# Optimization experiments

Hardware: AMD Instinct MI355X
Metric: run time of the kernel (lower is better)

The kernel has to match this reference:

```python
import jax, jax.numpy as jnp
import numpy as np


def setup_inputs() -> dict:
    key = jax.random.key(0)
    kq, kk, kv = jax.random.split(key, 3)
    B, S, D = 4, 4096, 64
    q = jax.random.normal(kq, (B, S, D), dtype=jnp.float32)
    k = jax.random.normal(kk, (B, S, D), dtype=jnp.float32)
    v = jax.random.normal(kv, (B, S, D), dtype=jnp.float32)
    return {"q": q, "k": k, "v": v}


def reference(q, k, v):
    # Faithful math of the original blocked loop:
    #   output_i += exp(Q_i @ K_j^T) @ V_j, summed over all column blocks j
    # which is exactly unnormalized exponential attention:
    #   out = exp(Q K^T) V  (no 1/sqrt(d) scaling, no softmax normalization,
    #   no max-subtraction -- matching the source module's math).
    scores = jnp.einsum("bqd,bkd->bqk", q, k)  # [B, Sq, Sk]
    return jnp.einsum("bqk,bkd->bqd", jnp.exp(scores), v)  # [B, Sq, D]
```

## Files before the change

kernel.cpp:

```cpp
#include <hip/hip_runtime.h>
#include <hip/hip_bf16.h>


typedef short    s16x4 __attribute__((ext_vector_type(4)));
typedef short    s16x8 __attribute__((ext_vector_type(8)));
typedef _Float16 h16x8 __attribute__((ext_vector_type(8)));
typedef float    fx4   __attribute__((ext_vector_type(4)));
typedef float    fx16  __attribute__((ext_vector_type(16)));

constexpr int S = 4096, D = 64, BN = 128;
constexpr int TILES = S / BN;
constexpr int HALF_TILES = TILES / 2;
constexpr int TILE_SHORTS  = 16 * 512;
constexpr int BATCH_SHORTS = TILES * TILE_SHORTS;

__device__ __forceinline__ unsigned short f2bf(float x) {
    unsigned u = __float_as_uint(x);
    u = (u + 0x7FFFu + ((u >> 16) & 1u)) >> 16;
    return (unsigned short)u;
}
__device__ __forceinline__ float bf2f(unsigned short h) {
    return __uint_as_float(((unsigned)h) << 16);
}
__device__ __forceinline__ unsigned short f2h(float x) {
    union { _Float16 h; unsigned short s; } u;
    u.h = (_Float16)x;
    return u.s;
}
__device__ __forceinline__ unsigned pack_bf16(float lo, float hi) {
    __hip_bfloat162 r = __float22bfloat162_rn(make_float2(lo, hi));
    union { __hip_bfloat162 b; unsigned u; } c;
    c.b = r;
    return c.u;
}
__device__ __forceinline__ float ex2(float x) {
#if __has_builtin(__builtin_amdgcn_exp2f)
    return __builtin_amdgcn_exp2f(x);
#else
    return exp2f(x);
#endif
}

__global__ __launch_bounds__(256) void prep2(
    const float* __restrict__ k, const float* __restrict__ v,
    unsigned short* __restrict__ kf, unsigned short* __restrict__ vf)
{
    __shared__ unsigned short tile[128 * 72];
    const int tid   = threadIdx.x;
    const int which = blockIdx.x & 1;
    const int t     = (blockIdx.x >> 1) & 31;
    const int b     = blockIdx.x >> 6;
    const float* src = (which ? v : k) + ((size_t)b * S + t * BN) * D;

    #pragma unroll
    for (int i = 0; i < 8; ++i) {
        int f   = i * 256 + tid;
        int row = f >> 4;
        int c4  = (f & 15) << 2;
        float4 x = *(const float4*)(src + row * D + c4);
        s16x4 o;
        if (which) o = (s16x4){(short)f2bf(x.x), (short)f2bf(x.y),
                               (short)f2bf(x.z), (short)f2bf(x.w)};
        else       o = (s16x4){(short)f2h(x.x), (short)f2h(x.y),
                               (short)f2h(x.z), (short)f2h(x.w)};
        *(s16x4*)&tile[row * 72 + c4] = o;
    }
    __syncthreads();

    const int lane = tid & 63;
    unsigned short* dst = (which ? vf : kf) + (size_t)b * BATCH_SHORTS + t * TILE_SHORTS;
    #pragma unroll
    for (int i = 0; i < 4; ++i) {
        int c = (tid >> 6) * 4 + i;
        s16x8 o;
        if (which == 0) {
            int row = (c >> 2) * 32 + (lane & 31);
            int dc  = (c & 3) * 16 + (lane >> 5) * 8;
            o = *(const s16x8*)&tile[row * 72 + dc];
        } else {
            int r0 = (c >> 1) * 16 + (lane >> 5) * 8;
            int dc = (c & 1) * 32 + (lane & 31);
            #pragma unroll
            for (int j = 0; j < 8; ++j) o[j] = (short)tile[(r0 + j) * 72 + dc];
        }
        *(s16x8*)(dst + c * 512 + lane * 8) = o;
    }
}

__global__ __launch_bounds__(512) void attn_main10(
    const float* __restrict__ q, const unsigned short* __restrict__ kf,
    const unsigned short* __restrict__ vf, float* __restrict__ partial)
{
    const int tid = threadIdx.x, lane = tid & 63, w = tid >> 6;
    const int h = lane >> 5, m5 = lane & 31;
    const int bid = blockIdx.x;
    const int kslice = bid & 7;
    const int kh = kslice >> 2;
    const int kkq = kslice & 3;
    const int rest = bid >> 3;
    const int b = rest & 3;
    const int q0 = (rest >> 2) * 512 + w * 64;
    const int t0 = kh * HALF_TILES;

    const unsigned short* kwb = kf + (size_t)b * BATCH_SHORTS + kkq * 4 * 512 + lane * 8;
    const unsigned short* vwb = vf + (size_t)b * BATCH_SHORTS + kkq * 4 * 512 + lane * 8;

    const float LOG2E = 1.4426950408889634f;
    h16x8 qf[2][4];
    #pragma unroll
    for (int mt = 0; mt < 2; ++mt) {
        const float* qrow = q + ((size_t)b * S + q0 + mt * 32 + m5) * D + h * 8;
        #pragma unroll
        for (int ks = 0; ks < 4; ++ks) {
            float4 a = *(const float4*)(qrow + ks * 16);
            float4 c = *(const float4*)(qrow + ks * 16 + 4);
            qf[mt][ks] = (h16x8){
                (_Float16)(a.x * LOG2E), (_Float16)(a.y * LOG2E),
                (_Float16)(a.z * LOG2E), (_Float16)(a.w * LOG2E),
                (_Float16)(c.x * LOG2E), (_Float16)(c.y * LOG2E),
                (_Float16)(c.z * LOG2E), (_Float16)(c.w * LOG2E)};
        }
    }

    fx16 oacc[2][2] = {};

    h16x8 kA0[4], kA1[4];
    s16x8 vB0[4], vB1[4];

    auto loadKV = [&](int t, h16x8* kA, s16x8* vB) {
        const unsigned short* kt = kwb + (size_t)t * TILE_SHORTS;
        const unsigned short* vt = vwb + (size_t)t * TILE_SHORTS;
        #pragma unroll
        for (int c = 0; c < 4; ++c) {
            kA[c] = *(const h16x8*)(kt + c * 512);
            vB[c] = *(const s16x8*)(vt + c * 512);
        }
    };

    auto computeTile = [&](const h16x8* kA, const s16x8* vB) {
        fx16 sa[2] = {};
        #pragma unroll
        for (int ks = 0; ks < 4; ++ks)
            #pragma unroll
            for (int mt = 0; mt < 2; ++mt)
                sa[mt] = __builtin_amdgcn_mfma_f32_32x32x16_f16(kA[ks], qf[mt][ks], sa[mt], 0, 0, 0);

        unsigned p01[2][8];
        #pragma unroll
        for (int mt = 0; mt < 2; ++mt)
            #pragma unroll
            for (int rp = 0; rp < 8; ++rp)
                p01[mt][rp] = pack_bf16(ex2(sa[mt][2 * rp]), ex2(sa[mt][2 * rp + 1]));

        union frag { unsigned u[4]; s16x8 v; };
        frag A[2][2];
        #pragma unroll
        for (int mt = 0; mt < 2; ++mt) {
#if __has_builtin(__builtin_amdgcn_permlane32_swap)
            typedef unsigned uix2 __attribute__((ext_vector_type(2)));
            uix2 r0 = __builtin_amdgcn_permlane32_swap(p01[mt][0], p01[mt][2], false, false);
            uix2 r1 = __builtin_amdgcn_permlane32_swap(p01[mt][1], p01[mt][3], false, false);
            A[mt][0].u[0] = r0.x; A[mt][0].u[1] = r1.x;
            A[mt][0].u[2] = r0.y; A[mt][0].u[3] = r1.y;
            uix2 r2 = __builtin_amdgcn_permlane32_swap(p01[mt][4], p01[mt][6], false, false);
            uix2 r3 = __builtin_amdgcn_permlane32_swap(p01[mt][5], p01[mt][7], false, false);
            A[mt][1].u[0] = r2.x; A[mt][1].u[1] = r3.x;
            A[mt][1].u[2] = r2.y; A[mt][1].u[3] = r3.y;
#else
            unsigned sw[8];
            #pragma unroll
            for (int rp = 0; rp < 8; ++rp)
                sw[rp] = (unsigned)__shfl_xor((int)p01[mt][rp], 32, 64);
            A[mt][0].u[0] = h ? sw[2]        : p01[mt][0];
            A[mt][0].u[1] = h ? sw[3]        : p01[mt][1];
            A[mt][0].u[2] = h ? p01[mt][2]   : sw[0];
            A[mt][0].u[3] = h ? p01[mt][3]   : sw[1];
            A[mt][1].u[0] = h ? sw[6]        : p01[mt][4];
            A[mt][1].u[1] = h ? sw[7]        : p01[mt][5];
            A[mt][1].u[2] = h ? p01[mt][6]   : sw[4];
            A[mt][1].u[3] = h ? p01[mt][7]   : sw[5];
#endif
        }

        #pragma unroll
        for (int u = 0; u < 2; ++u)
            #pragma unroll
            for (int dt = 0; dt < 2; ++dt)
                #pragma unroll
                for (int mt = 0; mt < 2; ++mt)
                    oacc[mt][dt] = __builtin_amdgcn_mfma_f32_32x32x16_bf16(
                        A[mt][u].v, vB[u * 2 + dt], oacc[mt][dt], 0, 0, 0);
    };

    loadKV(t0, kA0, vB0);
    for (int i = 0; i < HALF_TILES; i += 2) {
        if (i + 1 < HALF_TILES) loadKV(t0 + i + 1, kA1, vB1);
        computeTile(kA0, vB0);
        if (i + 2 < HALF_TILES) loadKV(t0 + i + 2, kA0, vB0);
        computeTile(kA1, vB1);
    }

    float* pout = partial + (((size_t)(kh * 4 + kkq)) * 4 + b) * S * D;
    #pragma unroll
    for (int dt = 0; dt < 2; ++dt)
        #pragma unroll
        for (int mt = 0; mt < 2; ++mt)
            #pragma unroll
            for (int r = 0; r < 16; ++r) {
                int row = q0 + mt * 32 + (r & 3) + 8 * (r >> 2) + 4 * h;
                pout[(size_t)row * D + dt * 32 + m5] = oacc[mt][dt][r];
            }
}

__global__ __launch_bounds__(256) void reduce_out8(
    const float4* __restrict__ p, float4* __restrict__ o, int n4)
{
    int i = blockIdx.x * 256 + threadIdx.x;
    if (i < n4) {
        float4 a = p[i];
        #pragma unroll
        for (int j = 1; j < 8; ++j) {
            float4 x = p[(size_t)j * n4 + i];
            a.x += x.x; a.y += x.y; a.z += x.z; a.w += x.w;
        }
        o[i] = a;
    }
}

__global__ __launch_bounds__(1024) void attn_fallback(
    const float* __restrict__ q, const float* __restrict__ k,
    const float* __restrict__ v, float* __restrict__ out)
{
    __shared__ unsigned short Kh[64][72];
    __shared__ unsigned short Kl[64][72];
    __shared__ unsigned short Vt[64][68];
    __shared__ unsigned short Pf[64][72];

    const int tid = threadIdx.x, lane = tid & 63, wave = tid >> 6;
    const int quad = lane >> 4, tq = lane & 15;
    const int kkb = wave & 3, mba = wave >> 2;
    const int b = blockIdx.y, q0 = blockIdx.x * 64;
    const float* qb = q + (size_t)b * S * D;
    const float* kb = k + (size_t)b * S * D;
    const float* vb = v + (size_t)b * S * D;
    float* ob = out + (size_t)b * S * D;

    s16x8 qh[2], ql[2];
    {
        const float* qrow = qb + (size_t)(q0 + mba * 16 + tq) * D;
        #pragma unroll
        for (int ks = 0; ks < 2; ++ks) {
            const float* src = qrow + ks * 32 + quad * 8;
            float4 f0 = *(const float4*)src;
            float4 f1 = *(const float4*)(src + 4);
            float f[8] = {f0.x, f0.y, f0.z, f0.w, f1.x, f1.y, f1.z, f1.w};
            #pragma unroll
            for (int j = 0; j < 8; ++j) {
                unsigned short hh = f2bf(f[j]);
                qh[ks][j] = (short)hh;
                ql[ks][j] = (short)f2bf(f[j] - bf2f(hh));
            }
        }
    }
    fx4 oacc = {0.f, 0.f, 0.f, 0.f};
    const int krow = tid >> 4, kc4 = (tid & 15) << 2;
    const int vd = tid & 63, vk = (tid >> 6) << 2;

    for (int t = 0; t < S / 64; ++t) {
        __syncthreads();
        const float* kt = kb + (size_t)(t * 64 + krow) * D;
        const float* vt = vb + (size_t)(t * 64 + vk) * D;
        {
            float4 kv = *(const float4*)(kt + kc4);
            unsigned short h0 = f2bf(kv.x), h1 = f2bf(kv.y), h2 = f2bf(kv.z), h3 = f2bf(kv.w);
            s16x4 a = {(short)h0, (short)h1, (short)h2, (short)h3};
            s16x4 l4 = {(short)f2bf(kv.x - bf2f(h0)), (short)f2bf(kv.y - bf2f(h1)),
                        (short)f2bf(kv.z - bf2f(h2)), (short)f2bf(kv.w - bf2f(h3))};
            *(s16x4*)&Kh[krow][kc4] = a;
            *(s16x4*)&Kl[krow][kc4] = l4;
            const float* vs = vt + vd;
            s16x4 vv = {(short)f2bf(vs[0]), (short)f2bf(vs[D]),
                        (short)f2bf(vs[2 * D]), (short)f2bf(vs[3 * D])};
            *(s16x4*)&Vt[vd][vk] = vv;
        }
        __syncthreads();
        fx4 sacc = {0.f, 0.f, 0.f, 0.f};
        #pragma unroll
        for (int ks = 0; ks < 2; ++ks) {
            s16x8 kah = *(const s16x8*)&Kh[kkb * 16 + tq][ks * 32 + quad * 8];
            s16x8 kal = *(const s16x8*)&Kl[kkb * 16 + tq][ks * 32 + quad * 8];
            sacc = __builtin_amdgcn_mfma_f32_16x16x32_bf16(kah, qh[ks], sacc, 0, 0, 0);
            sacc = __builtin_amdgcn_mfma_f32_16x16x32_bf16(kah, ql[ks], sacc, 0, 0, 0);
            sacc = __builtin_amdgcn_mfma_f32_16x16x32_bf16(kal, qh[ks], sacc, 0, 0, 0);
        }
        s16x4 pp = {(short)f2bf(__expf(sacc[0])), (short)f2bf(__expf(sacc[1])),
                    (short)f2bf(__expf(sacc[2])), (short)f2bf(__expf(sacc[3]))};
        *(s16x4*)&Pf[mba * 16 + tq][kkb * 16 + (quad << 2)] = pp;
        __syncthreads();
        #pragma unroll
        for (int ks = 0; ks < 2; ++ks) {
            s16x8 pa = *(const s16x8*)&Pf[mba * 16 + tq][ks * 32 + quad * 8];
            const unsigned short* vr = &Vt[kkb * 16 + tq][ks * 32 + quad * 8];
            s16x4 va = *(const s16x4*)vr;
            s16x4 vb2 = *(const s16x4*)(vr + 4);
            s16x8 vfull = __builtin_shufflevector(va, vb2, 0, 1, 2, 3, 4, 5, 6, 7);
            oacc = __builtin_amdgcn_mfma_f32_16x16x32_bf16(pa, vfull, oacc, 0, 0, 0);
        }
    }
    #pragma unroll
    for (int r = 0; r < 4; ++r)
        ob[(size_t)(q0 + mba * 16 + quad * 4 + r) * D + kkb * 16 + tq] = oacc[r];
}

extern "C" void kernel_launch(void* const* d_in, const int* in_sizes, int n_in,
                              void* d_out, int out_size, void* d_ws, size_t ws_size,
                              hipStream_t stream) {
    const float* q = (const float*)d_in[0];
    const float* k = (const float*)d_in[1];
    const float* v = (const float*)d_in[2];
    float* out = (float*)d_out;
    const int nbatch = in_sizes[0] / (S * D);
    const size_t elems = (size_t)nbatch * S * D;

    const size_t need = elems * 2 * 2 + elems * 8 * 4;
    if (nbatch == 4 && ws_size >= need && d_ws != nullptr) {
        unsigned short* kf = (unsigned short*)d_ws;
        unsigned short* vf = kf + elems;
        float* partial = (float*)(vf + elems);

        prep2<<<nbatch * TILES * 2, 256, 0, stream>>>(k, v, kf, vf);
        attn_main10<<<256, 512, 0, stream>>>(q, kf, vf, partial);
        const int n4 = (int)(elems / 4);
        reduce_out8<<<(n4 + 255) / 256, 256, 0, stream>>>(
            (const float4*)partial, (float4*)out, n4);
    } else {
        dim3 grid(S / 64, nbatch);
        attn_fallback<<<grid, 1024, 0, stream>>>(q, k, v, out);
    }
}
```

Baseline: 96.65 us.

## Fuse split-K partial reduction into attention kernel via atomic completion counters

Drops the separate reduce kernel. Each wave bumps an atomic counter for its 64-row output region after writing its partial, and the last of the 8 k-slices sums all partials and writes the final output. The counters are zeroed in the prep kernel. This removes one kernel launch and a full pass over the partial buffer, but the reduction now runs serially on a single wave per region at the tail of the main kernel, with extra fences.

```diff
diff --git a/kernel.cpp b/kernel.cpp
--- a/kernel.cpp
+++ b/kernel.cpp
@@ -43,10 +43,12 @@
 
 __global__ __launch_bounds__(256) void prep2(
     const float* __restrict__ k, const float* __restrict__ v,
-    unsigned short* __restrict__ kf, unsigned short* __restrict__ vf)
+    unsigned short* __restrict__ kf, unsigned short* __restrict__ vf,
+    unsigned* __restrict__ cnt)
 {
     __shared__ unsigned short tile[128 * 72];
     const int tid   = threadIdx.x;
+    if (blockIdx.x == 0) cnt[tid] = 0;
     const int which = blockIdx.x & 1;
     const int t     = (blockIdx.x >> 1) & 31;
     const int b     = blockIdx.x >> 6;
@@ -87,9 +89,10 @@
     }
 }
 
-__global__ __launch_bounds__(512) void attn_main10(
+__global__ __launch_bounds__(512) void attn_main11(
     const float* __restrict__ q, const unsigned short* __restrict__ kf,
-    const unsigned short* __restrict__ vf, float* __restrict__ partial)
+    const unsigned short* __restrict__ vf, float* __restrict__ partial,
+    unsigned* __restrict__ cnt, float* __restrict__ out)
 {
     const int tid = threadIdx.x, lane = tid & 63, w = tid >> 6;
     const int h = lane >> 5, m5 = lane & 31;
@@ -200,7 +203,7 @@
         computeTile(kA1, vB1);
     }
 
-    float* pout = partial + (((size_t)(kh * 4 + kkq)) * 4 + b) * S * D;
+    float* pout = partial + ((size_t)kslice * 4 + b) * S * D;
     #pragma unroll
     for (int dt = 0; dt < 2; ++dt)
         #pragma unroll
@@ -210,20 +213,27 @@
                 int row = q0 + mt * 32 + (r & 3) + 8 * (r >> 2) + 4 * h;
                 pout[(size_t)row * D + dt * 32 + m5] = oacc[mt][dt][r];
             }
-}
-
-__global__ __launch_bounds__(256) void reduce_out8(
-    const float4* __restrict__ p, float4* __restrict__ o, int n4)
-{
-    int i = blockIdx.x * 256 + threadIdx.x;
-    if (i < n4) {
-        float4 a = p[i];
-        #pragma unroll
-        for (int j = 1; j < 8; ++j) {
-            float4 x = p[(size_t)j * n4 + i];
-            a.x += x.x; a.y += x.y; a.z += x.z; a.w += x.w;
-        }
-        o[i] = a;
+
+    __threadfence();
+    const int region = ((q0 >> 6) << 2) + b;
+    unsigned old = 0;
+    if (lane == 0) old = atomicAdd(&cnt[region], 1u);
+    old = (unsigned)__shfl((int)old, 0, 64);
+    if (old == 7u) {
+        __threadfence();
+        const size_t roff = ((size_t)b * S + q0) * D / 4;
+        const size_t cstride = (size_t)4 * S * D / 4;
+        const float4* pb = (const float4*)partial;
+        float4* og = (float4*)out;
+        for (int i = lane; i < 1024; i += 64) {
+            float4 s = pb[roff + i];
+            #pragma unroll
+            for (int j = 1; j < 8; ++j) {
+                float4 x = pb[(size_t)j * cstride + roff + i];
+                s.x += x.x; s.y += x.y; s.z += x.z; s.w += x.w;
+            }
+            og[roff + i] = s;
+        }
     }
 }
 
@@ -322,17 +332,15 @@
     const int nbatch = in_sizes[0] / (S * D);
     const size_t elems = (size_t)nbatch * S * D;
 
-    const size_t need = elems * 2 * 2 + elems * 8 * 4;
+    const size_t need = elems * 2 * 2 + elems * 8 * 4 + 256 * 4;
     if (nbatch == 4 && ws_size >= need && d_ws != nullptr) {
         unsigned short* kf = (unsigned short*)d_ws;
         unsigned short* vf = kf + elems;
         float* partial = (float*)(vf + elems);
-
-        prep2<<<nbatch * TILES * 2, 256, 0, stream>>>(k, v, kf, vf);
-        attn_main10<<<256, 512, 0, stream>>>(q, kf, vf, partial);
-        const int n4 = (int)(elems / 4);
-        reduce_out8<<<(n4 + 255) / 256, 256, 0, stream>>>(
-            (const float4*)partial, (float4*)out, n4);
+        unsigned* cnt = (unsigned*)(partial + 8 * elems);
+
+        prep2<<<nbatch * TILES * 2, 256, 0, stream>>>(k, v, kf, vf, cnt);
+        attn_main11<<<256, 512, 0, stream>>>(q, kf, vf, partial, cnt, out);
     } else {
         dim3 grid(S / 64, nbatch);
         attn_fallback<<<grid, 1024, 0, stream>>>(q, k, v, out);
```

New measurement: 191.7 us. +98.4%, slower.
